# Kernel optimization log

Measured on AMD Instinct MI355X. Metric: run time of the kernel, lower is better.

## Reference

```python
import jax, jax.numpy as jnp
import numpy as np

GROUPS = 8
EPS = 1e-5


def _conv1x1(v, w, b):
    # v: (B,Ci,D,H,W), w: (Co,Ci), b: (Co,)
    return jnp.einsum('bidhw,oi->bodhw', v, w) + b[None, :, None, None, None]


def _spectral_conv(v, w1, w2, w3, w4):
    # v: (B,C,D,H,W); wk: (C,C,m,m,m,2) real/imag pairs
    B, C, D, H, W = v.shape
    m = w1.shape[2]
    xft = jnp.fft.rfftn(v, axes=(-3, -2, -1))  # (B,C,D,H,W//2+1) complex64

    def cmul(sub, wr):
        w = wr[..., 0] + 1j * wr[..., 1]
        return jnp.einsum('bixyz,ioxyz->boxyz', sub, w)

    out_ft = jnp.zeros((B, C, D, H, W // 2 + 1), jnp.complex64)
    out_ft = out_ft.at[:, :, :m, :m, :m].set(cmul(xft[:, :, :m, :m, :m], w1))
    out_ft = out_ft.at[:, :, -m:, :m, :m].set(cmul(xft[:, :, -m:, :m, :m], w2))
    out_ft = out_ft.at[:, :, :m, -m:, :m].set(cmul(xft[:, :, :m, -m:, :m], w3))
    out_ft = out_ft.at[:, :, -m:, -m:, :m].set(cmul(xft[:, :, -m:, -m:, :m], w4))
    return jnp.fft.irfftn(out_ft, s=(D, H, W), axes=(-3, -2, -1))


def _group_norm(s, g, b):
    # s: (B,C,D,H,W); per-channel affine g,b: (C,)
    B, C, D, H, W = s.shape
    x = s.reshape(B, GROUPS, C // GROUPS, D, H, W)
    mu = x.mean(axis=(2, 3, 4, 5), keepdims=True)
    var = x.var(axis=(2, 3, 4, 5), keepdims=True)
    x = (x - mu) * jax.lax.rsqrt(var + EPS)
    x = x.reshape(B, C, D, H, W)
    return x * g[None, :, None, None, None] + b[None, :, None, None, None]


def setup_inputs() -> dict:
    key = jax.random.key(0)
    ks = jax.random.split(key, 16)
    B, Cin, Cout, C, L, D = 1, 4, 3, 64, 3, 64
    m, latdim = 12, 512
    sc_scale = 1.0 / (C * C)

    def n(k, shape, s):
        return (jax.random.normal(k, shape, jnp.float32) * s).astype(jnp.float32)

    return {
        'x': jax.random.normal(ks[0], (B, Cin, D, D, D), jnp.float32),
        'latent': jax.random.normal(ks[1], (B, latdim), jnp.float32),
        'lift_w': n(ks[2], (C, Cin), 0.3),
        'lift_b': jnp.zeros((C,), jnp.float32),
        'sc_w1': n(ks[3], (L, C, C, m, m, m, 2), sc_scale),
        'sc_w2': n(ks[4], (L, C, C, m, m, m, 2), sc_scale),
        'sc_w3': n(ks[5], (L, C, C, m, m, m, 2), sc_scale),
        'sc_w4': n(ks[6], (L, C, C, m, m, m, 2), sc_scale),
        'conv_w': n(ks[7], (L, C, C), 0.1),
        'conv_b': jnp.zeros((L, C), jnp.float32),
        'gn_g': jnp.ones((L, C), jnp.float32),
        'gn_b': jnp.zeros((L, C), jnp.float32),
        'p1_w': n(ks[8], (2 * C, C), 0.1),
        'p1_b': jnp.zeros((2 * C,), jnp.float32),
        'p2_w': n(ks[9], (Cout, 2 * C), 0.1),
        'p2_b': jnp.zeros((Cout,), jnp.float32),
        'c1_w': n(ks[10], (2 * latdim, latdim), 0.03),
        'c1_b': jnp.zeros((2 * latdim,), jnp.float32),
        'c2_w': n(ks[11], (C * 2 * L, 2 * latdim), 0.03),
        'c2_b': jnp.zeros((C * 2 * L,), jnp.float32),
    }


def reference(x, latent, lift_w, lift_b, sc_w1, sc_w2, sc_w3, sc_w4,
              conv_w, conv_b, gn_g, gn_b, p1_w, p1_b, p2_w, p2_b,
              c1_w, c1_b, c2_w, c2_b):
    B = x.shape[0]
    L = conv_w.shape[0]
    C = lift_w.shape[0]

    # FiLM conditioner: Linear -> GELU(exact) -> Linear, reshape to (B,L,C,2)
    h = jax.nn.gelu(latent @ c1_w.T + c1_b, approximate=False)
    film = (h @ c2_w.T + c2_b).reshape(B, L, C, 2)

    v = _conv1x1(x, lift_w, lift_b)  # lift to width
    for i in range(L):  # small fixed layer count
        x1 = _spectral_conv(v, sc_w1[i], sc_w2[i], sc_w3[i], sc_w4[i])
        x2 = _conv1x1(v, conv_w[i], conv_b[i])
        v = jax.nn.gelu(_group_norm(x1 + x2, gn_g[i], gn_b[i]), approximate=False)
        scale = film[:, i, :, 0][:, :, None, None, None]
        shift = film[:, i, :, 1][:, :, None, None, None]
        v = v * (1.0 + scale) + shift
    v = jax.nn.gelu(_conv1x1(v, p1_w, p1_b), approximate=False)
    return _conv1x1(v, p2_w, p2_b)
```

## Files before the change

kernel.cpp:

```cpp
#include <hip/hip_runtime.h>
#include <hip/hip_bf16.h>
#include <math.h>

#define NS 262144
#define TWO_PI 6.283185307179586f

__device__ __forceinline__ float gelu_(float x) {
    return 0.5f * x * (1.0f + erff(x * 0.70710678118654752f));
}

__global__ void k_film1(const float* __restrict__ latent, const float* __restrict__ w,
                        const float* __restrict__ b, float* __restrict__ h) {
    int j = blockIdx.x * 256 + threadIdx.x;
    if (j >= 1024) return;
    float acc = b[j];
    const float* wr = w + j * 512;
    for (int k = 0; k < 512; k++) acc += latent[k] * wr[k];
    h[j] = gelu_(acc);
}

__global__ void k_film2(const float* __restrict__ h, const float* __restrict__ w,
                        const float* __restrict__ b, float* __restrict__ film) {
    int j = blockIdx.x * 256 + threadIdx.x;
    if (j >= 384) return;
    float acc = b[j];
    const float* wr = w + j * 1024;
    for (int k = 0; k < 1024; k++) acc += h[k] * wr[k];
    film[j] = acc;
}

__global__ void k_lift(const float* __restrict__ x, float* __restrict__ v,
                       const float* __restrict__ lw, const float* __restrict__ lb) {
    __shared__ float W[256];
    __shared__ float B[64];
    if (threadIdx.x < 256) W[threadIdx.x] = lw[threadIdx.x];
    if (threadIdx.x < 64) B[threadIdx.x] = lb[threadIdx.x];
    __syncthreads();
    int s = blockIdx.x * 256 + threadIdx.x;
    float x0 = x[s], x1 = x[NS + s], x2 = x[2 * NS + s], x3 = x[3 * NS + s];
#pragma unroll
    for (int c = 0; c < 64; c++) {
        v[c * NS + s] = W[c * 4] * x0 + W[c * 4 + 1] * x1 + W[c * 4 + 2] * x2 + W[c * 4 + 3] * x3 + B[c];
    }
}

#define INIT_TW \
    __shared__ float2 tw[64]; \
    if (threadIdx.x < 64) { \
        float s_, c_; \
        sincosf(TWO_PI * (float)threadIdx.x * (1.0f / 64.0f), &s_, &c_); \
        tw[threadIdx.x] = make_float2(c_, s_); \
    } \
    __syncthreads();

__global__ void k_fwd_w(const float* __restrict__ v, float2* __restrict__ A) {
    INIT_TW
    int flat = blockIdx.x * 256 + threadIdx.x;
    int row = flat / 12, kw = flat - row * 12;
    const float* base = v + row * 64;
    float re = 0.f, im = 0.f;
#pragma unroll
    for (int w = 0; w < 64; w++) {
        float2 t = tw[(kw * w) & 63];
        float xv = base[w];
        re += xv * t.x;
        im -= xv * t.y;
    }
    A[flat] = make_float2(re, im);
}

__global__ void k_fwd_h(const float2* __restrict__ A, float2* __restrict__ B) {
    INIT_TW
    int flat = blockIdx.x * 256 + threadIdx.x;
    int cd = flat / 288;
    int r = flat - cd * 288;
    int kh = r / 12, kw = r - kh * 12;
    int khf = kh < 12 ? kh : kh + 40;
    const float2* base = A + cd * 768 + kw;
    float re = 0.f, im = 0.f;
    for (int h = 0; h < 64; h++) {
        float2 a = base[h * 12];
        float2 t = tw[(khf * h) & 63];
        re += a.x * t.x + a.y * t.y;
        im += a.y * t.x - a.x * t.y;
    }
    B[flat] = make_float2(re, im);
}

__global__ void k_fwd_d(const float2* __restrict__ B, float2* __restrict__ Xf) {
    INIT_TW
    int flat = blockIdx.x * 256 + threadIdx.x;
    int c = flat / 6912;
    int r = flat - c * 6912;
    int kd = r / 288;
    int r2 = r - kd * 288;
    int kdf = kd < 12 ? kd : kd + 40;
    const float2* base = B + c * 18432 + r2;
    float re = 0.f, im = 0.f;
    for (int d = 0; d < 64; d++) {
        float2 a = base[d * 288];
        float2 t = tw[(kdf * d) & 63];
        re += a.x * t.x + a.y * t.y;
        im += a.y * t.x - a.x * t.y;
    }
    Xf[flat] = make_float2(re, im);
}

__global__ void k_modemul(const float2* __restrict__ Xf, float2* __restrict__ Yf,
                          const float2* __restrict__ w1, const float2* __restrict__ w2,
                          const float2* __restrict__ w3, const float2* __restrict__ w4) {
    int flat = blockIdx.x * 256 + threadIdx.x;
    int o = flat / 6912;
    int mode = flat - o * 6912;
    int kd = mode / 288;
    int r2 = mode - kd * 288;
    int kh = r2 / 12, kw = r2 - kh * 12;
    const float2* wsel = (kd < 12) ? ((kh < 12) ? w1 : w3) : ((kh < 12) ? w2 : w4);
    int xi = kd < 12 ? kd : kd - 12;
    int yi = kh < 12 ? kh : kh - 12;
    const float2* wbase = wsel + (size_t)o * 1728 + xi * 144 + yi * 12 + kw;
    const float2* xbase = Xf + mode;
    float re = 0.f, im = 0.f;
    for (int i = 0; i < 64; i++) {
        float2 xv = xbase[i * 6912];
        float2 wv = wbase[(size_t)i * 110592];
        re += xv.x * wv.x - xv.y * wv.y;
        im += xv.x * wv.y + xv.y * wv.x;
    }
    Yf[flat] = make_float2(re, im);
}

__global__ void k_inv_d(const float2* __restrict__ Yf, float2* __restrict__ Zd) {
    INIT_TW
    int flat = blockIdx.x * 256 + threadIdx.x;
    int od = flat / 288;
    int r2 = flat - od * 288;
    int o = od >> 6, d = od & 63;
    const float2* base = Yf + o * 6912 + r2;
    float re = 0.f, im = 0.f;
    for (int kd = 0; kd < 24; kd++) {
        float2 z = base[kd * 288];
        int kdf = kd < 12 ? kd : kd + 40;
        float2 t = tw[(kdf * d) & 63];
        re += z.x * t.x - z.y * t.y;
        im += z.x * t.y + z.y * t.x;
    }
    Zd[flat] = make_float2(re, im);
}

__global__ void k_inv_h(const float2* __restrict__ Zd, float2* __restrict__ Zh) {
    INIT_TW
    int flat = blockIdx.x * 256 + threadIdx.x;
    int odh = flat / 12;
    int kw = flat - odh * 12;
    int od = odh >> 6, h = odh & 63;
    const float2* base = Zd + od * 288 + kw;
    float re = 0.f, im = 0.f;
    for (int kh = 0; kh < 24; kh++) {
        float2 z = base[kh * 12];
        int khf = kh < 12 ? kh : kh + 40;
        float2 t = tw[(khf * h) & 63];
        re += z.x * t.x - z.y * t.y;
        im += z.x * t.y + z.y * t.x;
    }
    Zh[flat] = make_float2(re, im);
}

__global__ void k_inv_w(const float2* __restrict__ Zh, float* __restrict__ x1) {
    INIT_TW
    int s = blockIdx.x * 256 + threadIdx.x;
    int row = s >> 6, w = s & 63;
    const float2* base = Zh + row * 12;
    float acc = base[0].x;
#pragma unroll
    for (int kw = 1; kw < 12; kw++) {
        float2 z = base[kw];
        float2 t = tw[(kw * w) & 63];
        acc += 2.0f * (z.x * t.x - z.y * t.y);
    }
    x1[s] = acc * (1.0f / 262144.0f);
}

__global__ void k_conv_add(const float* __restrict__ v, float* __restrict__ x1,
                           const float* __restrict__ w, const float* __restrict__ b) {
    __shared__ float Wl[4096];
    __shared__ float Bl[64];
    for (int i = threadIdx.x; i < 4096; i += 256) Wl[i] = w[i];
    if (threadIdx.x < 64) Bl[threadIdx.x] = b[threadIdx.x];
    __syncthreads();
    int s = blockIdx.x * 256 + threadIdx.x;
    float acc[64];
#pragma unroll
    for (int o = 0; o < 64; o++) acc[o] = 0.f;
    for (int i = 0; i < 64; i += 4) {
        float vi0 = v[i * NS + s];
        float vi1 = v[(i + 1) * NS + s];
        float vi2 = v[(i + 2) * NS + s];
        float vi3 = v[(i + 3) * NS + s];
#pragma unroll
        for (int o = 0; o < 64; o++) {
            float4 w4 = *(const float4*)&Wl[o * 64 + i];
            acc[o] += w4.x * vi0 + w4.y * vi1 + w4.z * vi2 + w4.w * vi3;
        }
    }
#pragma unroll
    for (int o = 0; o < 64; o++) x1[o * NS + s] += acc[o] + Bl[o];
}

__global__ void k_gn_stats(const float* __restrict__ x1, float* __restrict__ stats) {
    int g = blockIdx.x >> 8, j = blockIdx.x & 255;
    const float* base = x1 + ((size_t)g << 21) + j * 8192;
    float s = 0.f, s2 = 0.f;
    for (int k = 0; k < 32; k++) {
        float val = base[k * 256 + threadIdx.x];
        s += val;
        s2 += val * val;
    }
    for (int off = 32; off > 0; off >>= 1) {
        s += __shfl_down(s, off);
        s2 += __shfl_down(s2, off);
    }
    __shared__ float ls[4], ls2[4];
    int wid = threadIdx.x >> 6, lid = threadIdx.x & 63;
    if (lid == 0) { ls[wid] = s; ls2[wid] = s2; }
    __syncthreads();
    if (threadIdx.x == 0) {
        atomicAdd(&stats[g * 2], ls[0] + ls[1] + ls[2] + ls[3]);
        atomicAdd(&stats[g * 2 + 1], ls2[0] + ls2[1] + ls2[2] + ls2[3]);
    }
}

__global__ void k_gn_apply(const float* __restrict__ x1, float* __restrict__ v,
                           const float* __restrict__ stats, const float* __restrict__ gg,
                           const float* __restrict__ gb, const float* __restrict__ film) {
    int idx = blockIdx.x * 256 + threadIdx.x;
    int c = idx >> 18;
    int g = c >> 3;
    float mean = stats[g * 2] * (1.0f / 2097152.0f);
    float var = stats[g * 2 + 1] * (1.0f / 2097152.0f) - mean * mean;
    float inv = rsqrtf(var + 1e-5f);
    float y = (x1[idx] - mean) * inv * gg[c] + gb[c];
    y = gelu_(y);
    float sc = film[c * 2], sh = film[c * 2 + 1];
    v[idx] = y * (1.0f + sc) + sh;
}

__global__ void k_p1p2(const float* __restrict__ v, float* __restrict__ out,
                       const float* __restrict__ w1, const float* __restrict__ b1,
                       const float* __restrict__ w2, const float* __restrict__ b2) {
    __shared__ float W1[8192];
    __shared__ float B1[128];
    __shared__ float W2[384];
    for (int i = threadIdx.x; i < 8192; i += 256) W1[i] = w1[i];
    if (threadIdx.x < 128) B1[threadIdx.x] = b1[threadIdx.x];
    if (threadIdx.x < 384 - 256) {}
    for (int i = threadIdx.x; i < 384; i += 256) W2[i] = w2[i];
    __syncthreads();
    int s = blockIdx.x * 256 + threadIdx.x;
    float vv[64];
#pragma unroll
    for (int c = 0; c < 64; c++) vv[c] = v[c * NS + s];
    float a0 = b2[0], a1 = b2[1], a2 = b2[2];
    for (int j = 0; j < 128; j++) {
        float t = B1[j];
        const float* wr = &W1[j * 64];
#pragma unroll
        for (int c = 0; c < 64; c += 4) {
            float4 w4 = *(const float4*)&wr[c];
            t += w4.x * vv[c] + w4.y * vv[c + 1] + w4.z * vv[c + 2] + w4.w * vv[c + 3];
        }
        t = gelu_(t);
        a0 += t * W2[j];
        a1 += t * W2[128 + j];
        a2 += t * W2[256 + j];
    }
    out[s] = a0;
    out[NS + s] = a1;
    out[2 * NS + s] = a2;
}

extern "C" void kernel_launch(void* const* d_in, const int* in_sizes, int n_in,
                              void* d_out, int out_size, void* d_ws, size_t ws_size,
                              hipStream_t stream) {
    const float* x      = (const float*)d_in[0];
    const float* latent = (const float*)d_in[1];
    const float* lift_w = (const float*)d_in[2];
    const float* lift_b = (const float*)d_in[3];
    const float* sc_w1  = (const float*)d_in[4];
    const float* sc_w2  = (const float*)d_in[5];
    const float* sc_w3  = (const float*)d_in[6];
    const float* sc_w4  = (const float*)d_in[7];
    const float* conv_w = (const float*)d_in[8];
    const float* conv_b = (const float*)d_in[9];
    const float* gn_g   = (const float*)d_in[10];
    const float* gn_b   = (const float*)d_in[11];
    const float* p1_w   = (const float*)d_in[12];
    const float* p1_b   = (const float*)d_in[13];
    const float* p2_w   = (const float*)d_in[14];
    const float* p2_b   = (const float*)d_in[15];
    const float* c1_w   = (const float*)d_in[16];
    const float* c1_b   = (const float*)d_in[17];
    const float* c2_w   = (const float*)d_in[18];
    const float* c2_b   = (const float*)d_in[19];

    float* ws = (float*)d_ws;
    float*  v    = ws;
    float*  x1   = ws + 16777216;
    float2* A    = (float2*)(ws + 33554432);
    float2* Bc   = (float2*)(ws + 39845888);
    float2* Xf   = (float2*)(ws + 42205184);
    float2* Yf   = (float2*)(ws + 43089920);
    float*  hbuf = ws + 43974656;
    float*  film = ws + 43975680;
    float*  stats= ws + 43976064;

    hipMemsetAsync(stats, 0, 48 * sizeof(float), stream);
    k_film1<<<4, 256, 0, stream>>>(latent, c1_w, c1_b, hbuf);
    k_film2<<<2, 256, 0, stream>>>(hbuf, c2_w, c2_b, film);
    k_lift<<<1024, 256, 0, stream>>>(x, v, lift_w, lift_b);

    for (int l = 0; l < 3; l++) {
        size_t woff = (size_t)l * 64 * 64 * 1728;
        k_fwd_w<<<12288, 256, 0, stream>>>(v, A);
        k_fwd_h<<<4608, 256, 0, stream>>>(A, Bc);
        k_fwd_d<<<1728, 256, 0, stream>>>(Bc, Xf);
        k_modemul<<<1728, 256, 0, stream>>>(Xf, Yf,
            (const float2*)sc_w1 + woff, (const float2*)sc_w2 + woff,
            (const float2*)sc_w3 + woff, (const float2*)sc_w4 + woff);
        k_inv_d<<<4608, 256, 0, stream>>>(Yf, Bc);
        k_inv_h<<<12288, 256, 0, stream>>>(Bc, A);
        k_inv_w<<<65536, 256, 0, stream>>>(A, x1);
        k_conv_add<<<1024, 256, 0, stream>>>(v, x1, conv_w + l * 4096, conv_b + l * 64);
        k_gn_stats<<<2048, 256, 0, stream>>>(x1, stats + l * 16);
        k_gn_apply<<<65536, 256, 0, stream>>>(x1, v, stats + l * 16,
                                              gn_g + l * 64, gn_b + l * 64, film + l * 128);
    }
    k_p1p2<<<1024, 256, 0, stream>>>(v, (float*)d_out, p1_w, p1_b, p2_w, p2_b);
}
```

Baseline: 1.812 ms.

## Replace shared-memory twiddle tables with recurrences and fuse GN stats into conv

After: 1.791 ms. About the same (-1.2%).

```diff
diff --git a/kernel.cpp b/kernel.cpp
--- a/kernel.cpp
+++ b/kernel.cpp
@@ -3,10 +3,13 @@
 #include <math.h>
 
 #define NS 262144
-#define TWO_PI 6.283185307179586f
+#define STEP64 0.09817477042468103f
 
 __device__ __forceinline__ float gelu_(float x) {
     return 0.5f * x * (1.0f + erff(x * 0.70710678118654752f));
+}
+__device__ __forceinline__ float2 cmul_(float2 a, float2 b) {
+    return make_float2(a.x * b.x - a.y * b.y, a.x * b.y + a.y * b.x);
 }
 
 __global__ void k_film1(const float* __restrict__ latent, const float* __restrict__ w,
@@ -31,64 +34,58 @@
 
 __global__ void k_lift(const float* __restrict__ x, float* __restrict__ v,
                        const float* __restrict__ lw, const float* __restrict__ lb) {
-    __shared__ float W[256];
-    __shared__ float B[64];
-    if (threadIdx.x < 256) W[threadIdx.x] = lw[threadIdx.x];
-    if (threadIdx.x < 64) B[threadIdx.x] = lb[threadIdx.x];
-    __syncthreads();
     int s = blockIdx.x * 256 + threadIdx.x;
     float x0 = x[s], x1 = x[NS + s], x2 = x[2 * NS + s], x3 = x[3 * NS + s];
 #pragma unroll
     for (int c = 0; c < 64; c++) {
-        v[c * NS + s] = W[c * 4] * x0 + W[c * 4 + 1] * x1 + W[c * 4 + 2] * x2 + W[c * 4 + 3] * x3 + B[c];
-    }
-}
-
-#define INIT_TW \
-    __shared__ float2 tw[64]; \
-    if (threadIdx.x < 64) { \
-        float s_, c_; \
-        sincosf(TWO_PI * (float)threadIdx.x * (1.0f / 64.0f), &s_, &c_); \
-        tw[threadIdx.x] = make_float2(c_, s_); \
-    } \
-    __syncthreads();
+        float4 wc = *(const float4*)(lw + c * 4);
+        v[c * NS + s] = wc.x * x0 + wc.y * x1 + wc.z * x2 + wc.w * x3 + lb[c];
+    }
+}
 
 __global__ void k_fwd_w(const float* __restrict__ v, float2* __restrict__ A) {
-    INIT_TW
     int flat = blockIdx.x * 256 + threadIdx.x;
     int row = flat / 12, kw = flat - row * 12;
-    const float* base = v + row * 64;
-    float re = 0.f, im = 0.f;
-#pragma unroll
-    for (int w = 0; w < 64; w++) {
-        float2 t = tw[(kw * w) & 63];
-        float xv = base[w];
-        re += xv * t.x;
-        im -= xv * t.y;
+    const float4* base = (const float4*)(v + row * 64);
+    float sn, cn;
+    sincosf((float)kw * STEP64, &sn, &cn);
+    float2 st = make_float2(cn, -sn);
+    float2 t = make_float2(1.f, 0.f);
+    float re = 0.f, im = 0.f;
+#pragma unroll
+    for (int w4 = 0; w4 < 16; w4++) {
+        float4 xv = base[w4];
+        re += xv.x * t.x; im += xv.x * t.y; t = cmul_(t, st);
+        re += xv.y * t.x; im += xv.y * t.y; t = cmul_(t, st);
+        re += xv.z * t.x; im += xv.z * t.y; t = cmul_(t, st);
+        re += xv.w * t.x; im += xv.w * t.y; t = cmul_(t, st);
     }
     A[flat] = make_float2(re, im);
 }
 
 __global__ void k_fwd_h(const float2* __restrict__ A, float2* __restrict__ B) {
-    INIT_TW
     int flat = blockIdx.x * 256 + threadIdx.x;
     int cd = flat / 288;
     int r = flat - cd * 288;
     int kh = r / 12, kw = r - kh * 12;
     int khf = kh < 12 ? kh : kh + 40;
     const float2* base = A + cd * 768 + kw;
-    float re = 0.f, im = 0.f;
+    float sn, cn;
+    sincosf((float)khf * STEP64, &sn, &cn);
+    float2 st = make_float2(cn, -sn);
+    float2 t = make_float2(1.f, 0.f);
+    float re = 0.f, im = 0.f;
+#pragma unroll 8
     for (int h = 0; h < 64; h++) {
         float2 a = base[h * 12];
-        float2 t = tw[(khf * h) & 63];
-        re += a.x * t.x + a.y * t.y;
-        im += a.y * t.x - a.x * t.y;
+        re += a.x * t.x - a.y * t.y;
+        im += a.x * t.y + a.y * t.x;
+        t = cmul_(t, st);
     }
     B[flat] = make_float2(re, im);
 }
 
 __global__ void k_fwd_d(const float2* __restrict__ B, float2* __restrict__ Xf) {
-    INIT_TW
     int flat = blockIdx.x * 256 + threadIdx.x;
     int c = flat / 6912;
     int r = flat - c * 6912;
@@ -96,12 +93,17 @@
     int r2 = r - kd * 288;
     int kdf = kd < 12 ? kd : kd + 40;
     const float2* base = B + c * 18432 + r2;
-    float re = 0.f, im = 0.f;
+    float sn, cn;
+    sincosf((float)kdf * STEP64, &sn, &cn);
+    float2 st = make_float2(cn, -sn);
+    float2 t = make_float2(1.f, 0.f);
+    float re = 0.f, im = 0.f;
+#pragma unroll 8
     for (int d = 0; d < 64; d++) {
         float2 a = base[d * 288];
-        float2 t = tw[(kdf * d) & 63];
-        re += a.x * t.x + a.y * t.y;
-        im += a.y * t.x - a.x * t.y;
+        re += a.x * t.x - a.y * t.y;
+        im += a.x * t.y + a.y * t.x;
+        t = cmul_(t, st);
     }
     Xf[flat] = make_float2(re, im);
 }
@@ -131,63 +133,97 @@
 }
 
 __global__ void k_inv_d(const float2* __restrict__ Yf, float2* __restrict__ Zd) {
-    INIT_TW
     int flat = blockIdx.x * 256 + threadIdx.x;
     int od = flat / 288;
     int r2 = flat - od * 288;
     int o = od >> 6, d = od & 63;
     const float2* base = Yf + o * 6912 + r2;
-    float re = 0.f, im = 0.f;
-    for (int kd = 0; kd < 24; kd++) {
+    float sn, cn;
+    sincosf((float)d * STEP64, &sn, &cn);
+    float2 st = make_float2(cn, sn);
+    float2 t = make_float2(1.f, 0.f);
+    float re = 0.f, im = 0.f;
+#pragma unroll
+    for (int kd = 0; kd < 12; kd++) {
         float2 z = base[kd * 288];
-        int kdf = kd < 12 ? kd : kd + 40;
-        float2 t = tw[(kdf * d) & 63];
         re += z.x * t.x - z.y * t.y;
         im += z.x * t.y + z.y * t.x;
+        t = cmul_(t, st);
+    }
+    float s2, c2;
+    sincosf((float)((52 * d) & 63) * STEP64, &s2, &c2);
+    t = make_float2(c2, s2);
+#pragma unroll
+    for (int kd = 12; kd < 24; kd++) {
+        float2 z = base[kd * 288];
+        re += z.x * t.x - z.y * t.y;
+        im += z.x * t.y + z.y * t.x;
+        t = cmul_(t, st);
     }
     Zd[flat] = make_float2(re, im);
 }
 
 __global__ void k_inv_h(const float2* __restrict__ Zd, float2* __restrict__ Zh) {
-    INIT_TW
     int flat = blockIdx.x * 256 + threadIdx.x;
     int odh = flat / 12;
     int kw = flat - odh * 12;
     int od = odh >> 6, h = odh & 63;
     const float2* base = Zd + od * 288 + kw;
-    float re = 0.f, im = 0.f;
-    for (int kh = 0; kh < 24; kh++) {
+    float sn, cn;
+    sincosf((float)h * STEP64, &sn, &cn);
+    float2 st = make_float2(cn, sn);
+    float2 t = make_float2(1.f, 0.f);
+    float re = 0.f, im = 0.f;
+#pragma unroll
+    for (int kh = 0; kh < 12; kh++) {
         float2 z = base[kh * 12];
-        int khf = kh < 12 ? kh : kh + 40;
-        float2 t = tw[(khf * h) & 63];
         re += z.x * t.x - z.y * t.y;
         im += z.x * t.y + z.y * t.x;
+        t = cmul_(t, st);
+    }
+    float s2, c2;
+    sincosf((float)((52 * h) & 63) * STEP64, &s2, &c2);
+    t = make_float2(c2, s2);
+#pragma unroll
+    for (int kh = 12; kh < 24; kh++) {
+        float2 z = base[kh * 12];
+        re += z.x * t.x - z.y * t.y;
+        im += z.x * t.y + z.y * t.x;
+        t = cmul_(t, st);
     }
     Zh[flat] = make_float2(re, im);
 }
 
 __global__ void k_inv_w(const float2* __restrict__ Zh, float* __restrict__ x1) {
-    INIT_TW
-    int s = blockIdx.x * 256 + threadIdx.x;
-    int row = s >> 6, w = s & 63;
+    int idx = blockIdx.x * 256 + threadIdx.x;
+    int row = idx >> 4;
+    int w0 = (idx & 15) * 4;
     const float2* base = Zh + row * 12;
-    float acc = base[0].x;
+    float2 z0 = base[0];
+    float acc0 = z0.x, acc1 = z0.x, acc2 = z0.x, acc3 = z0.x;
+    float sn, cn;
+    sincosf((float)w0 * STEP64, &sn, &cn);
+    const float2 e1 = make_float2(0.99518472667219688f, 0.09801714032956060f);
+    float2 s0 = make_float2(cn, sn);
+    float2 s1 = cmul_(s0, e1);
+    float2 s2 = cmul_(s1, e1);
+    float2 s3 = cmul_(s2, e1);
+    float2 t0 = s0, t1 = s1, t2 = s2, t3 = s3;
 #pragma unroll
     for (int kw = 1; kw < 12; kw++) {
         float2 z = base[kw];
-        float2 t = tw[(kw * w) & 63];
-        acc += 2.0f * (z.x * t.x - z.y * t.y);
-    }
-    x1[s] = acc * (1.0f / 262144.0f);
+        acc0 += 2.f * (z.x * t0.x - z.y * t0.y); t0 = cmul_(t0, s0);
+        acc1 += 2.f * (z.x * t1.x - z.y * t1.y); t1 = cmul_(t1, s1);
+        acc2 += 2.f * (z.x * t2.x - z.y * t2.y); t2 = cmul_(t2, s2);
+        acc3 += 2.f * (z.x * t3.x - z.y * t3.y); t3 = cmul_(t3, s3);
+    }
+    const float sc = 1.0f / 262144.0f;
+    *(float4*)(x1 + row * 64 + w0) = make_float4(acc0 * sc, acc1 * sc, acc2 * sc, acc3 * sc);
 }
 
 __global__ void k_conv_add(const float* __restrict__ v, float* __restrict__ x1,
-                           const float* __restrict__ w, const float* __restrict__ b) {
-    __shared__ float Wl[4096];
-    __shared__ float Bl[64];
-    for (int i = threadIdx.x; i < 4096; i += 256) Wl[i] = w[i];
-    if (threadIdx.x < 64) Bl[threadIdx.x] = b[threadIdx.x];
-    __syncthreads();
+                           const float* __restrict__ w, const float* __restrict__ b,
+                           float* __restrict__ stats) {
     int s = blockIdx.x * 256 + threadIdx.x;
     float acc[64];
 #pragma unroll
@@ -199,34 +235,36 @@
         float vi3 = v[(i + 3) * NS + s];
 #pragma unroll
         for (int o = 0; o < 64; o++) {
-            float4 w4 = *(const float4*)&Wl[o * 64 + i];
+            float4 w4 = *(const float4*)(w + o * 64 + i);
             acc[o] += w4.x * vi0 + w4.y * vi1 + w4.z * vi2 + w4.w * vi3;
         }
     }
-#pragma unroll
-    for (int o = 0; o < 64; o++) x1[o * NS + s] += acc[o] + Bl[o];
-}
-
-__global__ void k_gn_stats(const float* __restrict__ x1, float* __restrict__ stats) {
-    int g = blockIdx.x >> 8, j = blockIdx.x & 255;
-    const float* base = x1 + ((size_t)g << 21) + j * 8192;
-    float s = 0.f, s2 = 0.f;
-    for (int k = 0; k < 32; k++) {
-        float val = base[k * 256 + threadIdx.x];
-        s += val;
-        s2 += val * val;
-    }
+    float gs[16];
+#pragma unroll
+    for (int g = 0; g < 16; g++) gs[g] = 0.f;
+#pragma unroll
+    for (int o = 0; o < 64; o++) {
+        float t = x1[o * NS + s] + acc[o] + b[o];
+        x1[o * NS + s] = t;
+        gs[(o >> 3) * 2] += t;
+        gs[(o >> 3) * 2 + 1] += t * t;
+    }
+#pragma unroll
     for (int off = 32; off > 0; off >>= 1) {
-        s += __shfl_down(s, off);
-        s2 += __shfl_down(s2, off);
-    }
-    __shared__ float ls[4], ls2[4];
-    int wid = threadIdx.x >> 6, lid = threadIdx.x & 63;
-    if (lid == 0) { ls[wid] = s; ls2[wid] = s2; }
+#pragma unroll
+        for (int g = 0; g < 16; g++) gs[g] += __shfl_down(gs[g], off);
+    }
+    __shared__ float red[4][16];
+    int wid = threadIdx.x >> 6;
+    if ((threadIdx.x & 63) == 0) {
+#pragma unroll
+        for (int g = 0; g < 16; g++) red[wid][g] = gs[g];
+    }
     __syncthreads();
-    if (threadIdx.x == 0) {
-        atomicAdd(&stats[g * 2], ls[0] + ls[1] + ls[2] + ls[3]);
-        atomicAdd(&stats[g * 2 + 1], ls2[0] + ls2[1] + ls2[2] + ls2[3]);
+    if (threadIdx.x < 16) {
+        atomicAdd(&stats[threadIdx.x],
+                  red[0][threadIdx.x] + red[1][threadIdx.x] +
+                  red[2][threadIdx.x] + red[3][threadIdx.x]);
     }
 }
 
@@ -248,31 +286,23 @@
 __global__ void k_p1p2(const float* __restrict__ v, float* __restrict__ out,
                        const float* __restrict__ w1, const float* __restrict__ b1,
                        const float* __restrict__ w2, const float* __restrict__ b2) {
-    __shared__ float W1[8192];
-    __shared__ float B1[128];
-    __shared__ float W2[384];
-    for (int i = threadIdx.x; i < 8192; i += 256) W1[i] = w1[i];
-    if (threadIdx.x < 128) B1[threadIdx.x] = b1[threadIdx.x];
-    if (threadIdx.x < 384 - 256) {}
-    for (int i = threadIdx.x; i < 384; i += 256) W2[i] = w2[i];
-    __syncthreads();
     int s = blockIdx.x * 256 + threadIdx.x;
     float vv[64];
 #pragma unroll
     for (int c = 0; c < 64; c++) vv[c] = v[c * NS + s];
     float a0 = b2[0], a1 = b2[1], a2 = b2[2];
     for (int j = 0; j < 128; j++) {
-        float t = B1[j];
-        const float* wr = &W1[j * 64];
+        float t = b1[j];
+        const float* wr = w1 + j * 64;
 #pragma unroll
         for (int c = 0; c < 64; c += 4) {
-            float4 w4 = *(const float4*)&wr[c];
+            float4 w4 = *(const float4*)(wr + c);
             t += w4.x * vv[c] + w4.y * vv[c + 1] + w4.z * vv[c + 2] + w4.w * vv[c + 3];
         }
         t = gelu_(t);
-        a0 += t * W2[j];
-        a1 += t * W2[128 + j];
-        a2 += t * W2[256 + j];
+        a0 += t * w2[j];
+        a1 += t * w2[128 + j];
+        a2 += t * w2[256 + j];
     }
     out[s] = a0;
     out[NS + s] = a1;
@@ -329,9 +359,9 @@
             (const float2*)sc_w3 + woff, (const float2*)sc_w4 + woff);
         k_inv_d<<<4608, 256, 0, stream>>>(Yf, Bc);
         k_inv_h<<<12288, 256, 0, stream>>>(Bc, A);
-        k_inv_w<<<65536, 256, 0, stream>>>(A, x1);
-        k_conv_add<<<1024, 256, 0, stream>>>(v, x1, conv_w + l * 4096, conv_b + l * 64);
-        k_gn_stats<<<2048, 256, 0, stream>>>(x1, stats + l * 16);
+        k_inv_w<<<16384, 256, 0, stream>>>(A, x1);
+        k_conv_add<<<1024, 256, 0, stream>>>(v, x1, conv_w + l * 4096, conv_b + l * 64,
+                                             stats + l * 16);
         k_gn_apply<<<65536, 256, 0, stream>>>(x1, v, stats + l * 16,
                                               gn_g + l * 64, gn_b + l * 64, film + l * 128);
     }
```
